# Kernel optimization log

Measured on AMD Instinct MI355X. Metric: run time of the kernel, lower is better.

## Reference

```python
import jax, jax.numpy as jnp
from jax import lax
import numpy as np

Bn, DM, HH, WW = 2, 192, 64, 64   # batch, d_model, H, W (H==W required by transpose-stack)
DI = 384   # d_inner = ssm_ratio * d_model
DS = 16    # ssm_d_state
ND = 4     # n_directions
CG = 12    # c_group
LN_EPS = 1e-5


def setup_inputs() -> dict:
    key = jax.random.key(0)
    k = jax.random.split(key, 16)
    w = lambda i, shape: jax.random.normal(k[i], shape, jnp.float32) * 0.05
    return {
        "x": jax.random.normal(k[0], (Bn, DM, HH, WW), jnp.float32),
        "in_proj_w": w(1, (DI, DM)),
        "dwconv_w": w(2, (DI, 1, 3, 3)),
        "dwconv_b": w(3, (DI,)),
        "x_down_w": w(4, (DS, DI)),
        "w_up_w": w(5, (CG * DI, DS)),
        "l_up_w": w(6, (ND * DI, DS)),
        "u_up_w": w(7, (ND * DI, DS)),
        "d_up_w": w(8, (ND * DI, DS)),
        "m_w": w(9, (ND,)),
        "grn_gamma": w(10, (DI,)),
        "grn_beta": w(11, (DI,)),
        "norm_w": 1.0 + w(12, (DI,)),
        "norm_b": w(13, (DI,)),
        "out_proj_w": w(14, (DM, DI)),
    }


def _conv1x1(w, x):
    return jnp.einsum('oc,bchw->bohw', w, x)


def _gate_recurrent(X, B, G1, G2, G3):
    # H[:, :, h, w] = B*X + G1*H[h-1,w-1] + G2*H[h,w-1] + G3*H[h+1,w-1]
    # sequential over width; vectorized over batch/channel/height via a column scan.
    def step(hprev, col):  # hprev: [B, C, H]
        xw, bw, g1w, g2w, g3w = col
        z = jnp.zeros_like(hprev[:, :, :1])
        up = jnp.concatenate([z, hprev[:, :, :-1]], axis=2)   # H[h-1, w-1]
        dn = jnp.concatenate([hprev[:, :, 1:], z], axis=2)    # H[h+1, w-1]
        h = bw * xw + g1w * up + g2w * hprev + g3w * dn
        return h, h

    cols = tuple(jnp.moveaxis(t, 3, 0) for t in (X, B, G1, G2, G3))  # [W, B, C, H]
    h0 = jnp.zeros(X.shape[:3], X.dtype)
    _, ys = lax.scan(step, h0, cols)
    return jnp.moveaxis(ys, 0, 3)  # [B, C, H, W]


def _normalize_w(Gl, Gm, Gr):
    gl, gm, gr = jax.nn.sigmoid(Gl), jax.nn.sigmoid(Gm), jax.nn.sigmoid(Gr)
    s = gl + gm + gr
    s = s.at[:, :, 0, :].set(gm[:, :, 0, :] + gr[:, :, 0, :])
    s = s.at[:, :, -1, :].set(gl[:, :, -1, :] + gm[:, :, -1, :])
    s = jnp.maximum(s, 1e-7)
    return gl / s, gm / s, gr / s


def reference(x, in_proj_w, dwconv_w, dwconv_b, x_down_w, w_up_w, l_up_w, u_up_w,
              d_up_w, m_w, grn_gamma, grn_beta, norm_w, norm_b, out_proj_w):
    Bsz = x.shape[0]
    # in_proj (1x1, no bias) + SiLU + depthwise 3x3 conv
    h = jax.nn.silu(_conv1x1(in_proj_w, x))
    h = lax.conv_general_dilated(h, dwconv_w, (1, 1), ((1, 1), (1, 1)),
                                 feature_group_count=DI) + dwconv_b[None, :, None, None]
    # forward_corev1
    xp = _conv1x1(x_down_w, h)            # [B, DS, H, W]
    ws = _conv1x1(w_up_w, xp)             # [B, 12*DI, H, W]
    Ls = _conv1x1(l_up_w, xp)             # [B, 4*DI, H, W]
    Us = _conv1x1(u_up_w, xp)
    Ds = _conv1x1(d_up_w, xp)
    hT = jnp.swapaxes(h, 2, 3)            # requires H==W
    xs = jnp.concatenate([h, hT, h[..., ::-1], hT[..., ::-1]], axis=1)  # [B, 4*DI, H, W]
    G1, G2, G3 = jnp.split(ws, 3, axis=1)
    g1, g2, g3 = _normalize_w(G1, G2, G3)
    out = _gate_recurrent(xs, Ls, g1, g2, g3)
    out = out * Us + xs * Ds
    # merge directions: view [B, 4, DI*H, W], 1x1 conv 4->1
    out = out.reshape(Bsz, ND, DI * HH, WW)
    y = jnp.einsum('d,bdxw->bxw', m_w, out).reshape(Bsz, DI, HH, WW)
    # LayerNorm2d over channel dim
    mu = y.mean(axis=1, keepdims=True)
    var = ((y - mu) ** 2).mean(axis=1, keepdims=True)
    y = (y - mu) * lax.rsqrt(var + LN_EPS) * norm_w[None, :, None, None] + norm_b[None, :, None, None]
    # GRN
    Gx = jnp.sqrt(jnp.sum(y * y, axis=(2, 3), keepdims=True))        # [B, C, 1, 1]
    Nx = Gx / (Gx.mean(axis=1, keepdims=True) + 1e-6)
    y = grn_gamma[None, :, None, None] * (y * Nx) + grn_beta[None, :, None, None] + y
    # out_proj (1x1, no bias)
    return _conv1x1(out_proj_w, y)
```

## Files before the change

### kernel.cpp

```cpp
#include <hip/hip_runtime.h>
#include <math.h>

#define Bn 2
#define DM 192
#define DI 384
#define DS 16
#define HH 64
#define WW 64
#define HW 4096
#define ND 4

typedef __attribute__((ext_vector_type(2))) float v2f;
union Q4 { float4 f4; v2f v2[2]; };

__device__ __forceinline__ float fastrcp(float x) { return __builtin_amdgcn_rcpf(x); }
__device__ __forceinline__ float fsig(float x) {
    return fastrcp(1.0f + __expf(-x));
}

__global__ __launch_bounds__(256, 3) void k_inproj(const float* __restrict__ x,
                                                   const float* __restrict__ w,
                                                   float* __restrict__ hpre) {
    int og = blockIdx.y, b = blockIdx.z;
    int p = blockIdx.x * 256 + threadIdx.x;
    const float* wr = w + (size_t)og * 16 * DM;
    const float* xb = x + (size_t)b * DM * HW + p;
    v2f acc[16];
#pragma unroll
    for (int j = 0; j < 16; ++j) acc[j] = (v2f){0.f, 0.f};
    for (int c = 0; c < DM; c += 4) {
        float x0 = xb[(size_t)(c + 0) * HW];
        float x1 = xb[(size_t)(c + 1) * HW];
        float x2 = xb[(size_t)(c + 2) * HW];
        float x3 = xb[(size_t)(c + 3) * HW];
        v2f xA = {x0, x1}, xB = {x2, x3};
#pragma unroll
        for (int j = 0; j < 16; ++j) {
            const v2f* wv = reinterpret_cast<const v2f*>(wr + j * DM + c);
            acc[j] = __builtin_elementwise_fma(wv[0], xA, acc[j]);
            acc[j] = __builtin_elementwise_fma(wv[1], xB, acc[j]);
        }
    }
    float* hb = hpre + (size_t)b * DI * HW + (size_t)(og * 16) * HW + p;
#pragma unroll
    for (int j = 0; j < 16; ++j) {
        float v = acc[j].x + acc[j].y;
        hb[(size_t)j * HW] = v * fastrcp(1.0f + __expf(-v));
    }
}

__global__ __launch_bounds__(256) void k_dwconv(const float* __restrict__ hpre,
                                                const float* __restrict__ w,
                                                const float* __restrict__ bias,
                                                float* __restrict__ h) {
    int c = blockIdx.y, b = blockIdx.z;
    int p = blockIdx.x * 256 + threadIdx.x;
    int i = p >> 6, j = p & 63;
    const float* wp = w + c * 9;
    const float* src = hpre + ((size_t)b * DI + c) * HW;
    float acc = bias[c];
#pragma unroll
    for (int di = -1; di <= 1; ++di) {
        int ii = i + di;
        if (ii < 0 || ii >= HH) continue;
#pragma unroll
        for (int dj = -1; dj <= 1; ++dj) {
            int jj = j + dj;
            if (jj < 0 || jj >= WW) continue;
            acc = fmaf(wp[(di + 1) * 3 + (dj + 1)], src[ii * WW + jj], acc);
        }
    }
    h[((size_t)b * DI + c) * HW + p] = acc;
}

__global__ __launch_bounds__(256) void k_xdown(const float* __restrict__ h,
                                               const float* __restrict__ w,
                                               float* __restrict__ xpt) {
    __shared__ float red[4][64][17];
    int tid = threadIdx.x;
    int px = tid & 63, cw = tid >> 6;
    int gp = blockIdx.x * 64 + px;
    int b = gp >> 12, p = gp & 4095;
    const float* hb = h + (size_t)b * DI * HW + p;
    int c0 = cw * 96;
    v2f a[16];
#pragma unroll
    for (int s = 0; s < 16; ++s) a[s] = (v2f){0.f, 0.f};
    for (int cc = 0; cc < 96; cc += 4) {
        float h0 = hb[(size_t)(c0 + cc + 0) * HW];
        float h1 = hb[(size_t)(c0 + cc + 1) * HW];
        float h2 = hb[(size_t)(c0 + cc + 2) * HW];
        float h3 = hb[(size_t)(c0 + cc + 3) * HW];
        v2f xA = {h0, h1}, xB = {h2, h3};
#pragma unroll
        for (int s = 0; s < 16; ++s) {
            const v2f* wv = reinterpret_cast<const v2f*>(w + (size_t)s * DI + c0 + cc);
            a[s] = __builtin_elementwise_fma(wv[0], xA, a[s]);
            a[s] = __builtin_elementwise_fma(wv[1], xB, a[s]);
        }
    }
#pragma unroll
    for (int s = 0; s < 16; ++s) red[cw][px][s] = a[s].x + a[s].y;
    __syncthreads();
    int sg = tid >> 6;
    float4 r;
    float* o = &r.x;
#pragma unroll
    for (int j = 0; j < 4; ++j) {
        int s = sg * 4 + j;
        o[j] = red[0][px][s] + red[1][px][s] + red[2][px][s] + red[3][px][s];
    }
    int hp = p >> 6, wp_ = p & 63;
    reinterpret_cast<float4*>(xpt)[(size_t)b * (HW * 4) + (wp_ * 4 + sg) * 64 + hp] = r;
}

__device__ __forceinline__ float dot16p(const v2f* __restrict__ W,
                                        const Q4& a0, const Q4& a1,
                                        const Q4& a2, const Q4& a3) {
    v2f t0 = W[0] * a0.v2[0];
    v2f t1 = W[1] * a0.v2[1];
    t0 = __builtin_elementwise_fma(W[2], a1.v2[0], t0);
    t1 = __builtin_elementwise_fma(W[3], a1.v2[1], t1);
    t0 = __builtin_elementwise_fma(W[4], a2.v2[0], t0);
    t1 = __builtin_elementwise_fma(W[5], a2.v2[1], t1);
    t0 = __builtin_elementwise_fma(W[6], a3.v2[0], t0);
    t1 = __builtin_elementwise_fma(W[7], a3.v2[1], t1);
    v2f t = t0 + t1;
    return t.x + t.y;
}

__global__ __launch_bounds__(256, 3) void k_scan(const float* __restrict__ h,
                                                 const float* __restrict__ xpt,
                                                 const float* __restrict__ wup,
                                                 const float* __restrict__ lup,
                                                 const float* __restrict__ uup,
                                                 const float* __restrict__ dup,
                                                 const float* __restrict__ mw,
                                                 float* __restrict__ y) {
    int c = blockIdx.x, b = blockIdx.y;
    int tid = threadIdx.x;
    int d = tid >> 6, hl = tid & 63;

    __shared__ float htile[64][65];
    __shared__ float acc[64][65];

    const float* hb = h + ((size_t)b * DI + c) * HW;
    for (int i = tid; i < HW; i += 256) {
        htile[i >> 6][i & 63] = hb[i];
        acc[i >> 6][i & 63] = 0.f;
    }

    int row = d * DI + c;
    const float* p1 = wup + (size_t)row * DS;
    const float* p2 = wup + (size_t)(4 * DI + row) * DS;
    const float* p3 = wup + (size_t)(8 * DI + row) * DS;
    const float* pL = lup + (size_t)row * DS;
    const float* pU = uup + (size_t)row * DS;
    const float* pD = dup + (size_t)row * DS;
    float md = mw[d];
    v2f w1p[8], w2p[8], w3p[8], wLp[8], wUp[8], wDp[8];
#pragma unroll
    for (int k = 0; k < 8; ++k) {
        w1p[k] = *reinterpret_cast<const v2f*>(p1 + 2 * k);
        w2p[k] = *reinterpret_cast<const v2f*>(p2 + 2 * k);
        w3p[k] = *reinterpret_cast<const v2f*>(p3 + 2 * k);
        wLp[k] = *reinterpret_cast<const v2f*>(pL + 2 * k);
        wUp[k] = md * *reinterpret_cast<const v2f*>(pU + 2 * k);
        wDp[k] = md * *reinterpret_cast<const v2f*>(pD + 2 * k);
    }

    int xstep = (d & 1) ? 65 : 1;
    int xbase = (d & 1) ? hl : hl * 65;
    if (d & 2) { xbase += xstep * 63; xstep = -xstep; }
    const float* xptr = &htile[0][0] + xbase;

    int upA = ((hl - 1) & 63) << 2;
    int dnA = ((hl + 1) & 63) << 2;
    bool isTop = (hl == 0), isBot = (hl == 63);

    float* accp = &acc[hl][0];

    const float4* xg = reinterpret_cast<const float4*>(xpt) + (size_t)b * (HW * 4) + hl;

#define LOADQ(R0, R1, R2, R3, wcol) { \
    const float4* pp_ = xg + (size_t)(wcol) * 256; \
    R0.f4 = pp_[0]; R1.f4 = pp_[64]; R2.f4 = pp_[128]; R3.f4 = pp_[192]; }

#define PREP(g1S, g2S, g3S, invS, LS, US, DvS, XS, R0, R1, R2, R3) { \
    g1S = dot16p(w1p, R0, R1, R2, R3); \
    g2S = dot16p(w2p, R0, R1, R2, R3); \
    g3S = dot16p(w3p, R0, R1, R2, R3); \
    LS  = dot16p(wLp, R0, R1, R2, R3); \
    US  = dot16p(wUp, R0, R1, R2, R3); \
    DvS = dot16p(wDp, R0, R1, R2, R3); \
    g1S = fsig(g1S); g2S = fsig(g2S); g3S = fsig(g3S); \
    float ss_ = g2S + (isTop ? 0.f : g1S) + (isBot ? 0.f : g3S); \
    invS = fastrcp(fmaxf(ss_, 1e-7f)); \
    XS = *xptr; xptr += xstep; }

#define COMB(g1S, g2S, g3S, invS, LS, US, DvS, XS) { \
    float upv_ = isTop ? 0.f : __int_as_float(upr); \
    float dnv_ = isBot ? 0.f : __int_as_float(dnr); \
    float hnew_ = fmaf(LS, XS, invS * fmaf(g1S, upv_, fmaf(g2S, hprev, g3S * dnv_))); \
    atomicAdd(accp, fmaf(hnew_, US, XS * DvS)); accp += 1; \
    hprev = hnew_; \
    upr = __builtin_amdgcn_ds_bpermute(upA, __float_as_int(hprev)); \
    dnr = __builtin_amdgcn_ds_bpermute(dnA, __float_as_int(hprev)); }

    Q4 A0, A1, A2, A3, B0, B1, B2, B3;
    float g1a, g2a, g3a, inva, La, Ua, Dva, Xa;
    float g1b, g2b, g3b, invb, Lb, Ub, Dvb, Xb;
    int upr, dnr;
    float hprev;

    LOADQ(A0, A1, A2, A3, 0);
    __syncthreads();

    PREP(g1a, g2a, g3a, inva, La, Ua, Dva, Xa, A0, A1, A2, A3);
    LOADQ(A0, A1, A2, A3, 1);
    hprev = La * Xa;
    atomicAdd(accp, fmaf(hprev, Ua, Xa * Dva)); accp += 1;
    upr = __builtin_amdgcn_ds_bpermute(upA, __float_as_int(hprev));
    dnr = __builtin_amdgcn_ds_bpermute(dnA, __float_as_int(hprev));
    LOADQ(B0, B1, B2, B3, 2);

    for (int w = 1; w < 63; w += 2) {
        PREP(g1b, g2b, g3b, invb, Lb, Ub, Dvb, Xb, A0, A1, A2, A3);
        LOADQ(A0, A1, A2, A3, w + 2);
        COMB(g1b, g2b, g3b, invb, Lb, Ub, Dvb, Xb);
        PREP(g1a, g2a, g3a, inva, La, Ua, Dva, Xa, B0, B1, B2, B3);
        int wn = (w + 3 < 64) ? w + 3 : 63;
        LOADQ(B0, B1, B2, B3, wn);
        COMB(g1a, g2a, g3a, inva, La, Ua, Dva, Xa);
    }
    PREP(g1b, g2b, g3b, invb, Lb, Ub, Dvb, Xb, A0, A1, A2, A3);
    {
        float upv_ = isTop ? 0.f : __int_as_float(upr);
        float dnv_ = isBot ? 0.f : __int_as_float(dnr);
        float hnew_ = fmaf(Lb, Xb, invb * fmaf(g1b, upv_, fmaf(g2b, hprev, g3b * dnv_)));
        atomicAdd(accp, fmaf(hnew_, Ub, Xb * Dvb));
    }
#undef LOADQ
#undef PREP
#undef COMB

    __syncthreads();
    float* yb = y + ((size_t)b * DI + c) * HW;
    for (int i = tid; i < HW; i += 256) yb[i] = acc[i >> 6][i & 63];
}

__global__ __launch_bounds__(256) void k_ln(float* __restrict__ y,
                                            const float* __restrict__ nw,
                                            const float* __restrict__ nb) {
    int lpx = threadIdx.x & 15, chunk = threadIdx.x >> 4;
    int gp = blockIdx.x * 16 + lpx;
    int b = gp >> 12, p = gp & 4095;
    float* yb = y + (size_t)b * DI * HW + p;

    float vv[24];
    float s = 0.f, s2 = 0.f;
#pragma unroll
    for (int ci = 0; ci < 24; ++ci) {
        float v = yb[(size_t)(chunk * 24 + ci) * HW];
        vv[ci] = v;
        s += v;
        s2 = fmaf(v, v, s2);
    }
    __shared__ float S[16][17], S2[16][17];
    S[chunk][lpx] = s;
    S2[chunk][lpx] = s2;
    __syncthreads();
    float ts = 0.f, ts2 = 0.f;
#pragma unroll
    for (int k = 0; k < 16; ++k) { ts += S[k][lpx]; ts2 += S2[k][lpx]; }
    float mu = ts * (1.0f / DI);
    float var = ts2 * (1.0f / DI) - mu * mu;
    float inv = rsqrtf(var + 1e-5f);
#pragma unroll
    for (int ci = 0; ci < 24; ++ci) {
        int cch = chunk * 24 + ci;
        float v = (vv[ci] - mu) * inv;
        yb[(size_t)cch * HW] = fmaf(v, nw[cch], nb[cch]);
    }
}

__global__ __launch_bounds__(256) void k_grnsum(const float* __restrict__ y,
                                                float* __restrict__ gx) {
    int c = blockIdx.x, b = blockIdx.y;
    const float* yb = y + ((size_t)b * DI + c) * HW;
    float s = 0.f;
#pragma unroll 4
    for (int i = threadIdx.x; i < HW; i += 256) {
        float v = yb[i];
        s = fmaf(v, v, s);
    }
#pragma unroll
    for (int o = 32; o > 0; o >>= 1) s += __shfl_down(s, o);
    __shared__ float red[4];
    int wid = threadIdx.x >> 6;
    if ((threadIdx.x & 63) == 0) red[wid] = s;
    __syncthreads();
    if (threadIdx.x == 0) gx[b * DI + c] = sqrtf(red[0] + red[1] + red[2] + red[3]);
}

__global__ __launch_bounds__(256) void k_grnscale(const float* __restrict__ gxv,
                                                  const float* __restrict__ gamma,
                                                  float* __restrict__ sc) {
    int b = blockIdx.x;
    const float* g = gxv + b * DI;
    int cidx = threadIdx.x;
    float gx0 = g[cidx];
    float gx1 = (cidx < DI - 256) ? g[cidx + 256] : 0.f;
    float s = gx0 + gx1;
#pragma unroll
    for (int o = 32; o > 0; o >>= 1) s += __shfl_down(s, o);
    __shared__ float red[4];
    __shared__ float meanv;
    int wid = threadIdx.x >> 6;
    if ((threadIdx.x & 63) == 0) red[wid] = s;
    __syncthreads();
    if (threadIdx.x == 0) meanv = (red[0] + red[1] + red[2] + red[3]) * (1.0f / DI);
    __syncthreads();
    float m = meanv + 1e-6f;
    sc[b * DI + cidx] = 1.0f + gamma[cidx] * (gx0 / m);
    if (cidx < DI - 256)
        sc[b * DI + cidx + 256] = 1.0f + gamma[cidx + 256] * (gx1 / m);
}

__global__ __launch_bounds__(256, 3) void k_outproj(const float* __restrict__ y,
                                                    const float* __restrict__ w,
                                                    const float* __restrict__ sc_all,
                                                    const float* __restrict__ beta,
                                                    float* __restrict__ out) {
    int og = blockIdx.y, b = blockIdx.z;
    int p = blockIdx.x * 256 + threadIdx.x;
    const float* wr = w + (size_t)og * 8 * DI;
    const float* scb = sc_all + b * DI;
    const float* yb = y + (size_t)b * DI * HW + p;
    v2f acc[8];
#pragma unroll
    for (int j = 0; j < 8; ++j) acc[j] = (v2f){0.f, 0.f};
    for (int c = 0; c < DI; c += 4) {
        float v0 = fmaf(yb[(size_t)(c + 0) * HW], scb[c + 0], beta[c + 0]);
        float v1 = fmaf(yb[(size_t)(c + 1) * HW], scb[c + 1], beta[c + 1]);
        float v2 = fmaf(yb[(size_t)(c + 2) * HW], scb[c + 2], beta[c + 2]);
        float v3 = fmaf(yb[(size_t)(c + 3) * HW], scb[c + 3], beta[c + 3]);
        v2f vA = {v0, v1}, vB = {v2, v3};
#pragma unroll
        for (int j = 0; j < 8; ++j) {
            const v2f* wv = reinterpret_cast<const v2f*>(wr + j * DI + c);
            acc[j] = __builtin_elementwise_fma(wv[0], vA, acc[j]);
            acc[j] = __builtin_elementwise_fma(wv[1], vB, acc[j]);
        }
    }
    float* ob = out + (size_t)b * DM * HW + (size_t)(og * 8) * HW + p;
#pragma unroll
    for (int j = 0; j < 8; ++j) ob[(size_t)j * HW] = acc[j].x + acc[j].y;
}

extern "C" void kernel_launch(void* const* d_in, const int* in_sizes, int n_in,
                              void* d_out, int out_size, void* d_ws, size_t ws_size,
                              hipStream_t stream) {
    (void)in_sizes; (void)n_in; (void)out_size; (void)ws_size;
    const float* x          = (const float*)d_in[0];
    const float* in_proj_w  = (const float*)d_in[1];
    const float* dwconv_w   = (const float*)d_in[2];
    const float* dwconv_b   = (const float*)d_in[3];
    const float* x_down_w   = (const float*)d_in[4];
    const float* w_up_w     = (const float*)d_in[5];
    const float* l_up_w     = (const float*)d_in[6];
    const float* u_up_w     = (const float*)d_in[7];
    const float* d_up_w     = (const float*)d_in[8];
    const float* m_w        = (const float*)d_in[9];
    const float* grn_gamma  = (const float*)d_in[10];
    const float* grn_beta   = (const float*)d_in[11];
    const float* norm_w     = (const float*)d_in[12];
    const float* norm_b     = (const float*)d_in[13];
    const float* out_proj_w = (const float*)d_in[14];

    float* ws = (float*)d_ws;
    const size_t NBIG = (size_t)Bn * DI * HW;
    float* hpre = ws;
    float* hbuf = ws + NBIG;
    float* xpt  = ws + 2 * NBIG;
    float* gx   = ws + 2 * NBIG + (size_t)Bn * HW * DS;
    float* sc   = gx + Bn * DI;
    float* y    = hpre;

    k_inproj<<<dim3(16, 24, 2), 256, 0, stream>>>(x, in_proj_w, hpre);
    k_dwconv<<<dim3(16, DI, Bn), 256, 0, stream>>>(hpre, dwconv_w, dwconv_b, hbuf);
    k_xdown<<<dim3(128), 256, 0, stream>>>(hbuf, x_down_w, xpt);
    k_scan<<<dim3(DI, Bn), 256, 0, stream>>>(hbuf, xpt, w_up_w, l_up_w, u_up_w,
                                             d_up_w, m_w, y);
    k_ln<<<dim3(512), 256, 0, stream>>>(y, norm_w, norm_b);
    k_grnsum<<<dim3(DI, Bn), 256, 0, stream>>>(y, gx);
    k_grnscale<<<dim3(Bn), 256, 0, stream>>>(gx, grn_gamma, sc);
    k_outproj<<<dim3(16, 24, 2), 256, 0, stream>>>(y, out_proj_w, sc, grn_beta,
                                                   (float*)d_out);
}
```

Baseline: 214.1 us.

## Process two scan directions per thread with packed-float math in k_scan

The scan kernel now runs 128 threads per block, and each thread handles two directions (d and d+2), which share the same xpt column loads. The projections for both directions are computed with packed v2f FMAs, so each loaded activation feeds two outputs. The two contributions are summed before a single shared-memory atomicAdd, which halves the atomics and the global xpt loads per useful output. In exchange, per-thread register pressure roughly doubles (96 v2f weights), occupancy drops (launch bounds 128,2), and the sequential chain per thread is longer.

```diff
diff --git a/kernel.cpp b/kernel.cpp
--- a/kernel.cpp
+++ b/kernel.cpp
@@ -114,22 +114,7 @@
     reinterpret_cast<float4*>(xpt)[(size_t)b * (HW * 4) + (wp_ * 4 + sg) * 64 + hp] = r;
 }
 
-__device__ __forceinline__ float dot16p(const v2f* __restrict__ W,
-                                        const Q4& a0, const Q4& a1,
-                                        const Q4& a2, const Q4& a3) {
-    v2f t0 = W[0] * a0.v2[0];
-    v2f t1 = W[1] * a0.v2[1];
-    t0 = __builtin_elementwise_fma(W[2], a1.v2[0], t0);
-    t1 = __builtin_elementwise_fma(W[3], a1.v2[1], t1);
-    t0 = __builtin_elementwise_fma(W[4], a2.v2[0], t0);
-    t1 = __builtin_elementwise_fma(W[5], a2.v2[1], t1);
-    t0 = __builtin_elementwise_fma(W[6], a3.v2[0], t0);
-    t1 = __builtin_elementwise_fma(W[7], a3.v2[1], t1);
-    v2f t = t0 + t1;
-    return t.x + t.y;
-}
-
-__global__ __launch_bounds__(256, 3) void k_scan(const float* __restrict__ h,
+__global__ __launch_bounds__(128, 2) void k_scan(const float* __restrict__ h,
                                                  const float* __restrict__ xpt,
                                                  const float* __restrict__ wup,
                                                  const float* __restrict__ lup,
@@ -139,114 +124,163 @@
                                                  float* __restrict__ y) {
     int c = blockIdx.x, b = blockIdx.y;
     int tid = threadIdx.x;
-    int d = tid >> 6, hl = tid & 63;
+    int wid = tid >> 6, hl = tid & 63;
+    int dA = wid, dB = wid + 2;
 
     __shared__ float htile[64][65];
     __shared__ float acc[64][65];
 
     const float* hb = h + ((size_t)b * DI + c) * HW;
-    for (int i = tid; i < HW; i += 256) {
+    for (int i = tid; i < HW; i += 128) {
         htile[i >> 6][i & 63] = hb[i];
         acc[i >> 6][i & 63] = 0.f;
     }
 
-    int row = d * DI + c;
-    const float* p1 = wup + (size_t)row * DS;
-    const float* p2 = wup + (size_t)(4 * DI + row) * DS;
-    const float* p3 = wup + (size_t)(8 * DI + row) * DS;
-    const float* pL = lup + (size_t)row * DS;
-    const float* pU = uup + (size_t)row * DS;
-    const float* pD = dup + (size_t)row * DS;
-    float md = mw[d];
-    v2f w1p[8], w2p[8], w3p[8], wLp[8], wUp[8], wDp[8];
-#pragma unroll
-    for (int k = 0; k < 8; ++k) {
-        w1p[k] = *reinterpret_cast<const v2f*>(p1 + 2 * k);
-        w2p[k] = *reinterpret_cast<const v2f*>(p2 + 2 * k);
-        w3p[k] = *reinterpret_cast<const v2f*>(p3 + 2 * k);
-        wLp[k] = *reinterpret_cast<const v2f*>(pL + 2 * k);
-        wUp[k] = md * *reinterpret_cast<const v2f*>(pU + 2 * k);
-        wDp[k] = md * *reinterpret_cast<const v2f*>(pD + 2 * k);
-    }
-
-    int xstep = (d & 1) ? 65 : 1;
-    int xbase = (d & 1) ? hl : hl * 65;
-    if (d & 2) { xbase += xstep * 63; xstep = -xstep; }
-    const float* xptr = &htile[0][0] + xbase;
-
-    int upA = ((hl - 1) & 63) << 2;
-    int dnA = ((hl + 1) & 63) << 2;
+    int rowA = dA * DI + c, rowB = dB * DI + c;
+    const float* a1 = wup + (size_t)rowA * DS;
+    const float* b1 = wup + (size_t)rowB * DS;
+    const float* a2 = wup + (size_t)(4 * DI + rowA) * DS;
+    const float* b2 = wup + (size_t)(4 * DI + rowB) * DS;
+    const float* a3 = wup + (size_t)(8 * DI + rowA) * DS;
+    const float* b3 = wup + (size_t)(8 * DI + rowB) * DS;
+    const float* aL = lup + (size_t)rowA * DS;
+    const float* bL = lup + (size_t)rowB * DS;
+    const float* aU = uup + (size_t)rowA * DS;
+    const float* bU = uup + (size_t)rowB * DS;
+    const float* aD = dup + (size_t)rowA * DS;
+    const float* bD = dup + (size_t)rowB * DS;
+    float mdA = mw[dA], mdB = mw[dB];
+    v2f w1p[16], w2p[16], w3p[16], wLp[16], wUp[16], wDp[16];
+#pragma unroll
+    for (int s = 0; s < 16; ++s) {
+        w1p[s] = (v2f){a1[s], b1[s]};
+        w2p[s] = (v2f){a2[s], b2[s]};
+        w3p[s] = (v2f){a3[s], b3[s]};
+        wLp[s] = (v2f){aL[s], bL[s]};
+        wUp[s] = (v2f){mdA * aU[s], mdB * bU[s]};
+        wDp[s] = (v2f){mdA * aD[s], mdB * bD[s]};
+    }
+
+    int stepA = wid ? 65 : 1;
+    int baseA = wid ? hl : hl * 65;
+    int stepB = -stepA;
+    int baseB = baseA + stepA * 63;
+    const float* xpa = &htile[0][0] + baseA;
+    const float* xpb = &htile[0][0] + baseB;
+
+    int upAd = ((hl - 1) & 63) << 2;
+    int dnAd = ((hl + 1) & 63) << 2;
     bool isTop = (hl == 0), isBot = (hl == 63);
 
     float* accp = &acc[hl][0];
 
     const float4* xg = reinterpret_cast<const float4*>(xpt) + (size_t)b * (HW * 4) + hl;
+
+    struct SState {
+        v2f g1, g2, g3, L, U, Dv;
+        float invA, invB, XA, XB;
+    };
+
+    float hprevA, hprevB;
+    int uprA, dnrA, uprB, dnrB;
+
+    auto prep = [&](const Q4& q0, const Q4& q1, const Q4& q2, const Q4& q3, SState& S) {
+        const float xv[16] = {q0.f4.x, q0.f4.y, q0.f4.z, q0.f4.w,
+                              q1.f4.x, q1.f4.y, q1.f4.z, q1.f4.w,
+                              q2.f4.x, q2.f4.y, q2.f4.z, q2.f4.w,
+                              q3.f4.x, q3.f4.y, q3.f4.z, q3.f4.w};
+        v2f g1 = {0.f, 0.f}, g2 = {0.f, 0.f}, g3 = {0.f, 0.f};
+        v2f L = {0.f, 0.f}, U = {0.f, 0.f}, Dv = {0.f, 0.f};
+#pragma unroll
+        for (int s = 0; s < 16; ++s) {
+            v2f xs = {xv[s], xv[s]};
+            g1 = __builtin_elementwise_fma(w1p[s], xs, g1);
+            g2 = __builtin_elementwise_fma(w2p[s], xs, g2);
+            g3 = __builtin_elementwise_fma(w3p[s], xs, g3);
+            L  = __builtin_elementwise_fma(wLp[s], xs, L);
+            U  = __builtin_elementwise_fma(wUp[s], xs, U);
+            Dv = __builtin_elementwise_fma(wDp[s], xs, Dv);
+        }
+        S.g1 = (v2f){fsig(g1.x), fsig(g1.y)};
+        S.g2 = (v2f){fsig(g2.x), fsig(g2.y)};
+        S.g3 = (v2f){fsig(g3.x), fsig(g3.y)};
+        S.L = L; S.U = U; S.Dv = Dv;
+        float sA = S.g2.x + (isTop ? 0.f : S.g1.x) + (isBot ? 0.f : S.g3.x);
+        float sB = S.g2.y + (isTop ? 0.f : S.g1.y) + (isBot ? 0.f : S.g3.y);
+        S.invA = fastrcp(fmaxf(sA, 1e-7f));
+        S.invB = fastrcp(fmaxf(sB, 1e-7f));
+        S.XA = *xpa; xpa += stepA;
+        S.XB = *xpb; xpb += stepB;
+    };
+
+    auto comb = [&](const SState& S) {
+        float upAv = isTop ? 0.f : __int_as_float(uprA);
+        float dnAv = isBot ? 0.f : __int_as_float(dnrA);
+        float upBv = isTop ? 0.f : __int_as_float(uprB);
+        float dnBv = isBot ? 0.f : __int_as_float(dnrB);
+        float hnA = fmaf(S.L.x, S.XA,
+                         S.invA * fmaf(S.g1.x, upAv, fmaf(S.g2.x, hprevA, S.g3.x * dnAv)));
+        float hnB = fmaf(S.L.y, S.XB,
+                         S.invB * fmaf(S.g1.y, upBv, fmaf(S.g2.y, hprevB, S.g3.y * dnBv)));
+        atomicAdd(accp, fmaf(hnA, S.U.x, S.XA * S.Dv.x) + fmaf(hnB, S.U.y, S.XB * S.Dv.y));
+        accp += 1;
+        hprevA = hnA; hprevB = hnB;
+        uprA = __builtin_amdgcn_ds_bpermute(upAd, __float_as_int(hnA));
+        dnrA = __builtin_amdgcn_ds_bpermute(dnAd, __float_as_int(hnA));
+        uprB = __builtin_amdgcn_ds_bpermute(upAd, __float_as_int(hnB));
+        dnrB = __builtin_amdgcn_ds_bpermute(dnAd, __float_as_int(hnB));
+    };
 
 #define LOADQ(R0, R1, R2, R3, wcol) { \
     const float4* pp_ = xg + (size_t)(wcol) * 256; \
     R0.f4 = pp_[0]; R1.f4 = pp_[64]; R2.f4 = pp_[128]; R3.f4 = pp_[192]; }
 
-#define PREP(g1S, g2S, g3S, invS, LS, US, DvS, XS, R0, R1, R2, R3) { \
-    g1S = dot16p(w1p, R0, R1, R2, R3); \
-    g2S = dot16p(w2p, R0, R1, R2, R3); \
-    g3S = dot16p(w3p, R0, R1, R2, R3); \
-    LS  = dot16p(wLp, R0, R1, R2, R3); \
-    US  = dot16p(wUp, R0, R1, R2, R3); \
-    DvS = dot16p(wDp, R0, R1, R2, R3); \
-    g1S = fsig(g1S); g2S = fsig(g2S); g3S = fsig(g3S); \
-    float ss_ = g2S + (isTop ? 0.f : g1S) + (isBot ? 0.f : g3S); \
-    invS = fastrcp(fmaxf(ss_, 1e-7f)); \
-    XS = *xptr; xptr += xstep; }
-
-#define COMB(g1S, g2S, g3S, invS, LS, US, DvS, XS) { \
-    float upv_ = isTop ? 0.f : __int_as_float(upr); \
-    float dnv_ = isBot ? 0.f : __int_as_float(dnr); \
-    float hnew_ = fmaf(LS, XS, invS * fmaf(g1S, upv_, fmaf(g2S, hprev, g3S * dnv_))); \
-    atomicAdd(accp, fmaf(hnew_, US, XS * DvS)); accp += 1; \
-    hprev = hnew_; \
-    upr = __builtin_amdgcn_ds_bpermute(upA, __float_as_int(hprev)); \
-    dnr = __builtin_amdgcn_ds_bpermute(dnA, __float_as_int(hprev)); }
-
     Q4 A0, A1, A2, A3, B0, B1, B2, B3;
-    float g1a, g2a, g3a, inva, La, Ua, Dva, Xa;
-    float g1b, g2b, g3b, invb, Lb, Ub, Dvb, Xb;
-    int upr, dnr;
-    float hprev;
+    SState Sa, Sb;
 
     LOADQ(A0, A1, A2, A3, 0);
     __syncthreads();
 
-    PREP(g1a, g2a, g3a, inva, La, Ua, Dva, Xa, A0, A1, A2, A3);
+    prep(A0, A1, A2, A3, Sa);
     LOADQ(A0, A1, A2, A3, 1);
-    hprev = La * Xa;
-    atomicAdd(accp, fmaf(hprev, Ua, Xa * Dva)); accp += 1;
-    upr = __builtin_amdgcn_ds_bpermute(upA, __float_as_int(hprev));
-    dnr = __builtin_amdgcn_ds_bpermute(dnA, __float_as_int(hprev));
+    hprevA = Sa.L.x * Sa.XA;
+    hprevB = Sa.L.y * Sa.XB;
+    atomicAdd(accp, fmaf(hprevA, Sa.U.x, Sa.XA * Sa.Dv.x) +
+                    fmaf(hprevB, Sa.U.y, Sa.XB * Sa.Dv.y));
+    accp += 1;
+    uprA = __builtin_amdgcn_ds_bpermute(upAd, __float_as_int(hprevA));
+    dnrA = __builtin_amdgcn_ds_bpermute(dnAd, __float_as_int(hprevA));
+    uprB = __builtin_amdgcn_ds_bpermute(upAd, __float_as_int(hprevB));
+    dnrB = __builtin_amdgcn_ds_bpermute(dnAd, __float_as_int(hprevB));
     LOADQ(B0, B1, B2, B3, 2);
 
     for (int w = 1; w < 63; w += 2) {
-        PREP(g1b, g2b, g3b, invb, Lb, Ub, Dvb, Xb, A0, A1, A2, A3);
+        prep(A0, A1, A2, A3, Sb);
         LOADQ(A0, A1, A2, A3, w + 2);
-        COMB(g1b, g2b, g3b, invb, Lb, Ub, Dvb, Xb);
-        PREP(g1a, g2a, g3a, inva, La, Ua, Dva, Xa, B0, B1, B2, B3);
+        comb(Sb);
+        prep(B0, B1, B2, B3, Sa);
         int wn = (w + 3 < 64) ? w + 3 : 63;
         LOADQ(B0, B1, B2, B3, wn);
-        COMB(g1a, g2a, g3a, inva, La, Ua, Dva, Xa);
-    }
-    PREP(g1b, g2b, g3b, invb, Lb, Ub, Dvb, Xb, A0, A1, A2, A3);
+        comb(Sa);
+    }
+    prep(A0, A1, A2, A3, Sb);
     {
-        float upv_ = isTop ? 0.f : __int_as_float(upr);
-        float dnv_ = isBot ? 0.f : __int_as_float(dnr);
-        float hnew_ = fmaf(Lb, Xb, invb * fmaf(g1b, upv_, fmaf(g2b, hprev, g3b * dnv_)));
-        atomicAdd(accp, fmaf(hnew_, Ub, Xb * Dvb));
+        float upAv = isTop ? 0.f : __int_as_float(uprA);
+        float dnAv = isBot ? 0.f : __int_as_float(dnrA);
+        float upBv = isTop ? 0.f : __int_as_float(uprB);
+        float dnBv = isBot ? 0.f : __int_as_float(dnrB);
+        float hnA = fmaf(Sb.L.x, Sb.XA,
+                         Sb.invA * fmaf(Sb.g1.x, upAv, fmaf(Sb.g2.x, hprevA, Sb.g3.x * dnAv)));
+        float hnB = fmaf(Sb.L.y, Sb.XB,
+                         Sb.invB * fmaf(Sb.g1.y, upBv, fmaf(Sb.g2.y, hprevB, Sb.g3.y * dnBv)));
+        atomicAdd(accp, fmaf(hnA, Sb.U.x, Sb.XA * Sb.Dv.x) +
+                        fmaf(hnB, Sb.U.y, Sb.XB * Sb.Dv.y));
     }
 #undef LOADQ
-#undef PREP
-#undef COMB
 
     __syncthreads();
     float* yb = y + ((size_t)b * DI + c) * HW;
-    for (int i = tid; i < HW; i += 256) yb[i] = acc[i >> 6][i & 63];
+    for (int i = tid; i < HW; i += 128) yb[i] = acc[i >> 6][i & 63];
 }
 
 __global__ __launch_bounds__(256) void k_ln(float* __restrict__ y,
@@ -390,7 +424,7 @@
     k_inproj<<<dim3(16, 24, 2), 256, 0, stream>>>(x, in_proj_w, hpre);
     k_dwconv<<<dim3(16, DI, Bn), 256, 0, stream>>>(hpre, dwconv_w, dwconv_b, hbuf);
     k_xdown<<<dim3(128), 256, 0, stream>>>(hbuf, x_down_w, xpt);
-    k_scan<<<dim3(DI, Bn), 256, 0, stream>>>(hbuf, xpt, w_up_w, l_up_w, u_up_w,
+    k_scan<<<dim3(DI, Bn), 128, 0, stream>>>(hbuf, xpt, w_up_w, l_up_w, u_up_w,
                                              d_up_w, m_w, y);
     k_ln<<<dim3(512), 256, 0, stream>>>(y, norm_w, norm_b);
     k_grnsum<<<dim3(DI, Bn), 256, 0, stream>>>(y, gx);
```

Result: slower. 269.5 us (+25.9%).

## Fold GRN scale and beta into out_proj weights; use scalar-FMA dots in scan

Applied to the files above, without the earlier changes.

Replaces the per-element GRN affine (y*sc+beta) inside out_proj with a prep kernel that builds per-batch weights scaled by the GRN factor plus a precomputed W·beta bias, so the out_proj inner loop only loads y and does FMAs. In the scan kernel the packed-v2f dot products become scalar FMA chains on weights broadcast from lane 0 through __shfl, which lets the compiler keep them wave-uniform and in scalar registers and frees VGPRs. The cost is an extra small kernel that writes a per-batch weight copy into the workspace, and a serial 384-step dot product per output row for the bias.

```diff
diff --git a/kernel.cpp b/kernel.cpp
--- a/kernel.cpp
+++ b/kernel.cpp
@@ -11,7 +11,6 @@
 #define ND 4
 
 typedef __attribute__((ext_vector_type(2))) float v2f;
-union Q4 { float4 f4; v2f v2[2]; };
 
 __device__ __forceinline__ float fastrcp(float x) { return __builtin_amdgcn_rcpf(x); }
 __device__ __forceinline__ float fsig(float x) {
@@ -114,20 +113,11 @@
     reinterpret_cast<float4*>(xpt)[(size_t)b * (HW * 4) + (wp_ * 4 + sg) * 64 + hp] = r;
 }
 
-__device__ __forceinline__ float dot16p(const v2f* __restrict__ W,
-                                        const Q4& a0, const Q4& a1,
-                                        const Q4& a2, const Q4& a3) {
-    v2f t0 = W[0] * a0.v2[0];
-    v2f t1 = W[1] * a0.v2[1];
-    t0 = __builtin_elementwise_fma(W[2], a1.v2[0], t0);
-    t1 = __builtin_elementwise_fma(W[3], a1.v2[1], t1);
-    t0 = __builtin_elementwise_fma(W[4], a2.v2[0], t0);
-    t1 = __builtin_elementwise_fma(W[5], a2.v2[1], t1);
-    t0 = __builtin_elementwise_fma(W[6], a3.v2[0], t0);
-    t1 = __builtin_elementwise_fma(W[7], a3.v2[1], t1);
-    v2f t = t0 + t1;
-    return t.x + t.y;
-}
+#define DOT16(W, q0, q1, q2, q3) \
+    fmaf(W[15], q3.w, fmaf(W[14], q3.z, fmaf(W[13], q3.y, fmaf(W[12], q3.x, \
+    fmaf(W[11], q2.w, fmaf(W[10], q2.z, fmaf(W[9],  q2.y, fmaf(W[8],  q2.x, \
+    fmaf(W[7],  q1.w, fmaf(W[6],  q1.z, fmaf(W[5],  q1.y, fmaf(W[4],  q1.x, \
+    fmaf(W[3],  q0.w, fmaf(W[2],  q0.z, fmaf(W[1],  q0.y, W[0] * q0.x)))))))))))))))
 
 __global__ __launch_bounds__(256, 3) void k_scan(const float* __restrict__ h,
                                                  const float* __restrict__ xpt,
@@ -158,15 +148,20 @@
     const float* pU = uup + (size_t)row * DS;
     const float* pD = dup + (size_t)row * DS;
     float md = mw[d];
-    v2f w1p[8], w2p[8], w3p[8], wLp[8], wUp[8], wDp[8];
-#pragma unroll
-    for (int k = 0; k < 8; ++k) {
-        w1p[k] = *reinterpret_cast<const v2f*>(p1 + 2 * k);
-        w2p[k] = *reinterpret_cast<const v2f*>(p2 + 2 * k);
-        w3p[k] = *reinterpret_cast<const v2f*>(p3 + 2 * k);
-        wLp[k] = *reinterpret_cast<const v2f*>(pL + 2 * k);
-        wUp[k] = md * *reinterpret_cast<const v2f*>(pU + 2 * k);
-        wDp[k] = md * *reinterpret_cast<const v2f*>(pD + 2 * k);
+    float w1[16], w2[16], w3[16], wL[16], wU[16], wD[16];
+#pragma unroll
+    for (int s = 0; s < 16; ++s) {
+        w1[s] = p1[s]; w2[s] = p2[s]; w3[s] = p3[s];
+        wL[s] = pL[s]; wU[s] = md * pU[s]; wD[s] = md * pD[s];
+    }
+#pragma unroll
+    for (int s = 0; s < 16; ++s) {
+        w1[s] = __shfl(w1[s], 0);
+        w2[s] = __shfl(w2[s], 0);
+        w3[s] = __shfl(w3[s], 0);
+        wL[s] = __shfl(wL[s], 0);
+        wU[s] = __shfl(wU[s], 0);
+        wD[s] = __shfl(wD[s], 0);
     }
 
     int xstep = (d & 1) ? 65 : 1;
@@ -184,15 +179,15 @@
 
 #define LOADQ(R0, R1, R2, R3, wcol) { \
     const float4* pp_ = xg + (size_t)(wcol) * 256; \
-    R0.f4 = pp_[0]; R1.f4 = pp_[64]; R2.f4 = pp_[128]; R3.f4 = pp_[192]; }
+    R0 = pp_[0]; R1 = pp_[64]; R2 = pp_[128]; R3 = pp_[192]; }
 
 #define PREP(g1S, g2S, g3S, invS, LS, US, DvS, XS, R0, R1, R2, R3) { \
-    g1S = dot16p(w1p, R0, R1, R2, R3); \
-    g2S = dot16p(w2p, R0, R1, R2, R3); \
-    g3S = dot16p(w3p, R0, R1, R2, R3); \
-    LS  = dot16p(wLp, R0, R1, R2, R3); \
-    US  = dot16p(wUp, R0, R1, R2, R3); \
-    DvS = dot16p(wDp, R0, R1, R2, R3); \
+    g1S = DOT16(w1, R0, R1, R2, R3); \
+    g2S = DOT16(w2, R0, R1, R2, R3); \
+    g3S = DOT16(w3, R0, R1, R2, R3); \
+    LS  = DOT16(wL, R0, R1, R2, R3); \
+    US  = DOT16(wU, R0, R1, R2, R3); \
+    DvS = DOT16(wD, R0, R1, R2, R3); \
     g1S = fsig(g1S); g2S = fsig(g2S); g3S = fsig(g3S); \
     float ss_ = g2S + (isTop ? 0.f : g1S) + (isBot ? 0.f : g3S); \
     invS = fastrcp(fmaxf(ss_, 1e-7f)); \
@@ -207,7 +202,7 @@
     upr = __builtin_amdgcn_ds_bpermute(upA, __float_as_int(hprev)); \
     dnr = __builtin_amdgcn_ds_bpermute(dnA, __float_as_int(hprev)); }
 
-    Q4 A0, A1, A2, A3, B0, B1, B2, B3;
+    float4 A0, A1, A2, A3, B0, B1, B2, B3;
     float g1a, g2a, g3a, inva, La, Ua, Dva, Xa;
     float g1b, g2b, g3b, invb, Lb, Ub, Dvb, Xb;
     int upr, dnr;
@@ -303,48 +298,64 @@
     if (threadIdx.x == 0) gx[b * DI + c] = sqrtf(red[0] + red[1] + red[2] + red[3]);
 }
 
-__global__ __launch_bounds__(256) void k_grnscale(const float* __restrict__ gxv,
-                                                  const float* __restrict__ gamma,
-                                                  float* __restrict__ sc) {
-    int b = blockIdx.x;
+__global__ __launch_bounds__(256) void k_wprep(const float* __restrict__ gxv,
+                                               const float* __restrict__ gamma,
+                                               const float* __restrict__ w,
+                                               const float* __restrict__ beta,
+                                               float* __restrict__ wsc,
+                                               float* __restrict__ wbeta) {
+    int b = blockIdx.y;
+    int tid = threadIdx.x;
     const float* g = gxv + b * DI;
-    int cidx = threadIdx.x;
-    float gx0 = g[cidx];
-    float gx1 = (cidx < DI - 256) ? g[cidx + 256] : 0.f;
-    float s = gx0 + gx1;
-#pragma unroll
-    for (int o = 32; o > 0; o >>= 1) s += __shfl_down(s, o);
+    __shared__ float scl[DI];
     __shared__ float red[4];
     __shared__ float meanv;
-    int wid = threadIdx.x >> 6;
-    if ((threadIdx.x & 63) == 0) red[wid] = s;
-    __syncthreads();
-    if (threadIdx.x == 0) meanv = (red[0] + red[1] + red[2] + red[3]) * (1.0f / DI);
+
+    float gx0 = g[tid];
+    float gx1 = (tid < DI - 256) ? g[tid + 256] : 0.f;
+    float s = gx0 + gx1;
+#pragma unroll
+    for (int o = 32; o > 0; o >>= 1) s += __shfl_down(s, o);
+    int wid = tid >> 6;
+    if ((tid & 63) == 0) red[wid] = s;
+    __syncthreads();
+    if (tid == 0) meanv = (red[0] + red[1] + red[2] + red[3]) * (1.0f / DI);
     __syncthreads();
     float m = meanv + 1e-6f;
-    sc[b * DI + cidx] = 1.0f + gamma[cidx] * (gx0 / m);
-    if (cidx < DI - 256)
-        sc[b * DI + cidx + 256] = 1.0f + gamma[cidx + 256] * (gx1 / m);
+    scl[tid] = 1.0f + gamma[tid] * (gx0 / m);
+    if (tid < DI - 256) scl[tid + 256] = 1.0f + gamma[tid + 256] * (gx1 / m);
+    __syncthreads();
+
+    int j0 = blockIdx.x * 24;
+    for (int i = tid; i < 24 * DI; i += 256) {
+        int j = j0 + (i / DI), cc = i - (i / DI) * DI;
+        wsc[((size_t)b * DM + j) * DI + cc] = w[(size_t)j * DI + cc] * scl[cc];
+    }
+    if (b == 0 && tid < 24) {
+        int j = j0 + tid;
+        const float* wj = w + (size_t)j * DI;
+        float sum = 0.f;
+        for (int cc = 0; cc < DI; ++cc) sum = fmaf(wj[cc], beta[cc], sum);
+        wbeta[j] = sum;
+    }
 }
 
 __global__ __launch_bounds__(256, 3) void k_outproj(const float* __restrict__ y,
-                                                    const float* __restrict__ w,
-                                                    const float* __restrict__ sc_all,
-                                                    const float* __restrict__ beta,
+                                                    const float* __restrict__ wsc,
+                                                    const float* __restrict__ wbeta,
                                                     float* __restrict__ out) {
     int og = blockIdx.y, b = blockIdx.z;
     int p = blockIdx.x * 256 + threadIdx.x;
-    const float* wr = w + (size_t)og * 8 * DI;
-    const float* scb = sc_all + b * DI;
+    const float* wr = wsc + ((size_t)b * DM + og * 8) * DI;
     const float* yb = y + (size_t)b * DI * HW + p;
     v2f acc[8];
 #pragma unroll
     for (int j = 0; j < 8; ++j) acc[j] = (v2f){0.f, 0.f};
     for (int c = 0; c < DI; c += 4) {
-        float v0 = fmaf(yb[(size_t)(c + 0) * HW], scb[c + 0], beta[c + 0]);
-        float v1 = fmaf(yb[(size_t)(c + 1) * HW], scb[c + 1], beta[c + 1]);
-        float v2 = fmaf(yb[(size_t)(c + 2) * HW], scb[c + 2], beta[c + 2]);
-        float v3 = fmaf(yb[(size_t)(c + 3) * HW], scb[c + 3], beta[c + 3]);
+        float v0 = yb[(size_t)(c + 0) * HW];
+        float v1 = yb[(size_t)(c + 1) * HW];
+        float v2 = yb[(size_t)(c + 2) * HW];
+        float v3 = yb[(size_t)(c + 3) * HW];
         v2f vA = {v0, v1}, vB = {v2, v3};
 #pragma unroll
         for (int j = 0; j < 8; ++j) {
@@ -355,7 +366,8 @@
     }
     float* ob = out + (size_t)b * DM * HW + (size_t)(og * 8) * HW + p;
 #pragma unroll
-    for (int j = 0; j < 8; ++j) ob[(size_t)j * HW] = acc[j].x + acc[j].y;
+    for (int j = 0; j < 8; ++j)
+        ob[(size_t)j * HW] = acc[j].x + acc[j].y + wbeta[og * 8 + j];
 }
 
 extern "C" void kernel_launch(void* const* d_in, const int* in_sizes, int n_in,
@@ -380,12 +392,13 @@
 
     float* ws = (float*)d_ws;
     const size_t NBIG = (size_t)Bn * DI * HW;
-    float* hpre = ws;
-    float* hbuf = ws + NBIG;
-    float* xpt  = ws + 2 * NBIG;
-    float* gx   = ws + 2 * NBIG + (size_t)Bn * HW * DS;
-    float* sc   = gx + Bn * DI;
-    float* y    = hpre;
+    float* hpre  = ws;
+    float* hbuf  = ws + NBIG;
+    float* xpt   = ws + 2 * NBIG;
+    float* gx    = ws + 2 * NBIG + (size_t)Bn * HW * DS;
+    float* y     = hpre;
+    float* wsc   = hbuf;
+    float* wbeta = hbuf + (size_t)Bn * DM * DI;
 
     k_inproj<<<dim3(16, 24, 2), 256, 0, stream>>>(x, in_proj_w, hpre);
     k_dwconv<<<dim3(16, DI, Bn), 256, 0, stream>>>(hpre, dwconv_w, dwconv_b, hbuf);
@@ -394,7 +407,7 @@
                                              d_up_w, m_w, y);
     k_ln<<<dim3(512), 256, 0, stream>>>(y, norm_w, norm_b);
     k_grnsum<<<dim3(DI, Bn), 256, 0, stream>>>(y, gx);
-    k_grnscale<<<dim3(Bn), 256, 0, stream>>>(gx, grn_gamma, sc);
-    k_outproj<<<dim3(16, 24, 2), 256, 0, stream>>>(y, out_proj_w, sc, grn_beta,
-                                                   (float*)d_out);
-}
+    k_wprep<<<dim3(8, Bn), 256, 0, stream>>>(gx, grn_gamma, out_proj_w, grn_beta,
+                                             wsc, wbeta);
+    k_outproj<<<dim3(16, 24, 2), 256, 0, stream>>>(y, wsc, wbeta, (float*)d_out);
+}
```

New measurement: 228.0 us. 1.07x slower.
